# Performance work log

Hardware: AMD Instinct MI355X
Metric: run time of the kernel (lower is better)

The kernel has to match this reference:

```python
import jax, jax.numpy as jnp
import numpy as np
import math

N, E, LAT, MUL, HD = 20000, 160000, 128, 16, 32
H = LAT // HD          # 4 heads
D = 9                  # 0e+1o+2e spherical harmonics dim
SLICES = ((0, 1), (1, 4), (4, 9))
TPD = MUL * len(SLICES)


def _mlp(x, W1, b1, W2, b2):
    return jnp.dot(jax.nn.silu(jnp.dot(x, W1) + b1), W2) + b2


def _eq_linear(x, W):
    # block-diagonal per-l channel mixing: x [E, mul, D], W [n_l, mul, mul]
    return jnp.concatenate([jnp.einsum('ji,eim->ejm', W[l], x[:, :, s:t])
                            for l, (s, t) in enumerate(SLICES)], axis=-1)


def _residual(x, x_new, uc):
    co = jax.lax.rsqrt(uc * uc + 1.0)
    return co * x + (uc * co) * x_new


def _vec_rej(feat, dirs):
    d = dirs[:, None, :]
    return feat - (feat * d).sum(-1, keepdims=True) * d


def _so3_ln(x, eps=1e-8):
    # equivariant RMS layernorm per irrep block
    out = []
    for s, t in SLICES:
        blk = x[:, :, s:t]
        rms = jnp.sqrt((blk * blk).sum(-1).mean(-1) + eps)  # [N]
        out.append(blk / rms[:, None, None])
    return jnp.concatenate(out, axis=-1)


def _ln(x, g, b, eps=1e-5):
    mu = x.mean(-1, keepdims=True)
    var = ((x - mu) ** 2).mean(-1, keepdims=True)
    return (x - mu) * jax.lax.rsqrt(var + eps) * g + b


def _forward(h, X, t_ij, spharms, update_coeff, Wtq, Wtk, Wrs_W, Wrs_b, Wq_W, Wq_b, Wk_W, Wk_b, Wre_W, ln_g, ln_b, Wvu,
             gs_W1, gs_b1, gs_W2, gs_b2, gv_W1, gv_b1, gv_W2, gv_b2, gw_W1, gw_b1, gw_W2, gw_b2,
             gt_W1, gt_b1, gt_W2, gt_b2, gsp_W1, gsp_b1, gsp_W2, gsp_b2, md_W1, md_b1, md_W2, md_b2,
             mt_W1, mt_b1, mt_W2, mt_b2, gm_W1, gm_b1, gm_W2, gm_b2,
             edge_center, edge_neighbor, num_nodes):
    uc = update_coeff
    Xn = X[edge_neighbor]                                     # [E, mul, D]
    Xq = _vec_rej(_eq_linear(X[edge_center], Wtq), spharms)
    Xk = _vec_rej(_eq_linear(Xn, Wtk), -spharms)
    # CG scalar contraction (l x l -> 0e, uuu): normalized per-l dot product
    w = jnp.concatenate([(Xq[:, :, s:t] * Xk[:, :, s:t]).sum(-1) / math.sqrt(t - s)
                         for s, t in SLICES], axis=-1)        # [E, 3*mul]
    dt = _mlp(w, gw_W1, gw_b1, gw_W2, gw_b2) * _mlp(t_ij, gt_W1, gt_b1, gt_W2, gt_b2)
    t_ij = _residual(t_ij, dt, uc)
    h_i = h[edge_center]
    h_j = h[edge_neighbor]
    spatial = (t_ij @ Wrs_W + Wrs_b) * _mlp(h_j, gs_W1, gs_b1, gs_W2, gs_b2)
    En = t_ij.shape[0]
    q = (h_i @ Wq_W + Wq_b).reshape(En, H, HD)
    k = (h_j @ Wk_W + Wk_b).reshape(En, H, HD)
    v = _mlp(h_j, gv_W1, gv_b1, gv_W2, gv_b2)
    ta = jax.nn.silu(t_ij @ Wre_W).reshape(En, H, HD)
    alpha = (q * k * ta).sum(-1) / math.sqrt(HD)              # [E, H]
    amax = jax.ops.segment_max(alpha, edge_center, num_segments=num_nodes)
    ex = jnp.exp(alpha - amax[edge_center])
    den = jax.ops.segment_sum(ex, edge_center, num_segments=num_nodes)
    attn = ex / den[edge_center]                              # scatter_softmax
    sea = (attn[:, :, None] * v.reshape(En, H, HD)).reshape(En, LAT)
    combined = sea + spatial
    gates = _mlp(combined, gsp_W1, gsp_b1, gsp_W2, gsp_b2)
    o_s, o_d, o_t = gates[:, :LAT], gates[:, LAT:2 * LAT], gates[:, 2 * LAT:]
    dh = _ln(jax.ops.segment_sum(o_s, edge_center, num_segments=num_nodes), ln_g, ln_b)
    h = _residual(h, dh, uc)
    gd = _mlp(o_d, md_W1, md_b1, md_W2, md_b2)
    gtt = _mlp(o_t, mt_W1, mt_b1, mt_W2, mt_b2)
    dXij = gd[:, :, None] * spharms[:, None, :] + gtt[:, :, None] * Xn
    dX = _so3_ln(jax.ops.segment_sum(dXij, edge_center, num_segments=num_nodes))
    X = _residual(X, dX, uc)
    # EQFF
    Xp = jnp.einsum('nmi,mj->nji', X, Wvu)
    nrm = jnp.sqrt((Xp * Xp).sum(-1) + 1e-12)
    g = _mlp(jnp.concatenate([h, nrm], axis=-1), gm_W1, gm_b1, gm_W2, gm_b2)
    h = h + g[:, :LAT]
    X = X + g[:, LAT:, None] * Xp
    return h, X, t_ij


def setup_inputs() -> dict:
    key = jax.random.key(0)
    ks = jax.random.split(key, 24)

    def mk_mlp(k, din, dout):
        k1, k2 = jax.random.split(k)
        return (jax.random.normal(k1, (din, LAT)) / math.sqrt(din), jnp.zeros((LAT,)),
                jax.random.normal(k2, (LAT, dout)) / math.sqrt(LAT), jnp.zeros((dout,)))

    inp = {
        'h': jax.random.normal(ks[0], (N, LAT)),
        'X': jax.random.normal(ks[1], (N, MUL, D)),
        't_ij': jax.random.normal(ks[2], (E, LAT)),
        'spharms': jax.random.normal(ks[3], (E, D)),
        'update_coeff': jnp.ones((1,), dtype=jnp.float32),
        'Wtq': jax.random.normal(ks[4], (len(SLICES), MUL, MUL)) / math.sqrt(MUL),
        'Wtk': jax.random.normal(ks[5], (len(SLICES), MUL, MUL)) / math.sqrt(MUL),
        'Wrs_W': jax.random.normal(ks[6], (LAT, LAT)) / math.sqrt(LAT),
        'Wrs_b': jnp.zeros((LAT,)),
        'Wq_W': jax.random.normal(ks[7], (LAT, LAT)) / math.sqrt(LAT),
        'Wq_b': jnp.zeros((LAT,)),
        'Wk_W': jax.random.normal(ks[8], (LAT, LAT)) / math.sqrt(LAT),
        'Wk_b': jnp.zeros((LAT,)),
        'Wre_W': jax.random.normal(ks[9], (LAT, LAT)) / math.sqrt(LAT),
        'ln_g': jnp.ones((LAT,)),
        'ln_b': jnp.zeros((LAT,)),
        'Wvu': jax.random.normal(ks[10], (MUL, MUL)) / math.sqrt(MUL),
    }
    for name, din, dout, k in [('gs', LAT, LAT, ks[11]), ('gv', LAT, LAT, ks[12]), ('gw', TPD, LAT, ks[13]),
                               ('gt', LAT, LAT, ks[14]), ('gsp', LAT, 3 * LAT, ks[15]), ('md', LAT, MUL, ks[16]),
                               ('mt', LAT, MUL, ks[17]), ('gm', LAT + MUL, LAT + MUL, ks[18])]:
        W1, b1, W2, b2 = mk_mlp(k, din, dout)
        inp[name + '_W1'], inp[name + '_b1'], inp[name + '_W2'], inp[name + '_b2'] = W1, b1, W2, b2
    inp['edge_center'] = jax.random.randint(ks[19], (E,), 0, N)
    inp['edge_neighbor'] = jax.random.randint(ks[20], (E,), 0, N)
    inp['num_nodes'] = N
    return inp


def reference(h, X, t_ij, spharms, update_coeff, Wtq, Wtk, Wrs_W, Wrs_b, Wq_W, Wq_b, Wk_W, Wk_b, Wre_W, ln_g, ln_b, Wvu,
              gs_W1, gs_b1, gs_W2, gs_b2, gv_W1, gv_b1, gv_W2, gv_b2, gw_W1, gw_b1, gw_W2, gw_b2,
              gt_W1, gt_b1, gt_W2, gt_b2, gsp_W1, gsp_b1, gsp_W2, gsp_b2, md_W1, md_b1, md_W2, md_b2,
              mt_W1, mt_b1, mt_W2, mt_b2, gm_W1, gm_b1, gm_W2, gm_b2,
              edge_center, edge_neighbor, num_nodes):
    return _forward(h, X, t_ij, spharms, update_coeff, Wtq, Wtk, Wrs_W, Wrs_b, Wq_W, Wq_b, Wk_W, Wk_b, Wre_W, ln_g, ln_b, Wvu,
                    gs_W1, gs_b1, gs_W2, gs_b2, gv_W1, gv_b1, gv_W2, gv_b2, gw_W1, gw_b1, gw_W2, gw_b2,
                    gt_W1, gt_b1, gt_W2, gt_b2, gsp_W1, gsp_b1, gsp_W2, gsp_b2, md_W1, md_b1, md_W2, md_b2,
                    mt_W1, mt_b1, mt_W2, mt_b2, gm_W1, gm_b1, gm_W2, gm_b2,
                    edge_center, edge_neighbor, num_nodes)
```

## Files before the change

kernel.cpp:

```cpp
#include <hip/hip_runtime.h>
#include <math.h>

#define N_NODES 20000
#define E_EDGES 160000
#define LAT 128
#define MUL 16
#define DD 9
#define TPD 48

#define WS_QB     ((size_t)0)
#define WS_KB     (WS_QB + (size_t)N_NODES*LAT/2)
#define WS_VB     (WS_KB + (size_t)N_NODES*LAT/2)
#define WS_SB     (WS_VB + (size_t)N_NODES*LAT/2)
#define WS_W48    (WS_SB + (size_t)N_NODES*LAT/2)
#define WS_SPATB  (WS_W48 + (size_t)E_EDGES*TPD)
#define WS_ALPHA  (WS_SPATB + (size_t)E_EDGES*LAT/2)
#define WS_ZERO   (WS_ALPHA + (size_t)E_EDGES*4)
#define WS_AMAX   WS_ZERO
#define WS_DEN    (WS_AMAX + (size_t)N_NODES*4)
#define WS_HSUM   (WS_DEN + (size_t)N_NODES*4)
#define WS_NDX    (WS_HSUM + (size_t)N_NODES*LAT/2)
#define WS_END    (WS_NDX + (size_t)N_NODES*72)
#define ZERO_CNT  (WS_END - WS_ZERO)
#define WS_WB     WS_END
#define WS_XB     (WS_WB + (size_t)145408)

#define WOFF_WQ   0
#define WOFF_WK   16384
#define WOFF_GV1  32768
#define WOFF_GV2  49152
#define WOFF_GS1  65536
#define WOFF_GS2  81920
#define WOFF_GW1  98304
#define WOFF_GW2  106496
#define WOFF_GT1  122880
#define WOFF_GT2  139264
#define WOFF_WRS  155648
#define WOFF_WRE  172032
#define WOFF_GSP1 188416
#define WOFF_GSP2 204800
#define WOFF_MD1  253952
#define WOFF_MD2  270336
#define WOFF_MT1  272384
#define WOFF_MT2  288768
#define WB_TOTAL  290816

#define PREP_ZB   11250
#define PREP_PB   1136
#define PREP_XB   5625
#define K1B       (N_NODES/32)
#define K2B       (E_EDGES/16)

#define DEVI __device__ __forceinline__

typedef short short8 __attribute__((ext_vector_type(8)));
typedef float f32x4 __attribute__((ext_vector_type(4)));

DEVI float silu_f(float x){ return x / (1.f + __expf(-x)); }
DEVI unsigned int fmap(float x){ unsigned int b=__float_as_uint(x); return (b&0x80000000u)? ~b : (b|0x80000000u); }
DEVI float funmap(unsigned int u){ return (u&0x80000000u)? __uint_as_float(u&0x7fffffffu) : __uint_as_float(~u); }

DEVI unsigned short f2b(float f){ unsigned int u=__float_as_uint(f); return (unsigned short)((u + 0x7fffu + ((u>>16)&1u))>>16); }
DEVI unsigned int f2b2(float lo, float hi){ return ((unsigned int)f2b(hi)<<16) | (unsigned int)f2b(lo); }
DEVI float b2f(unsigned short u){ return __uint_as_float(((unsigned int)u)<<16); }

DEVI void atom_pk(unsigned short* p, unsigned int pk){
  asm volatile("global_atomic_pk_add_bf16 %0, %1, off" :: "v"(p), "v"(pk) : "memory");
}

DEVI f32x4 mfma16(short8 a, short8 b, f32x4 c){
  return __builtin_amdgcn_mfma_f32_16x16x32_bf16(a,b,c,0,0,0);
}

template<int KB>
DEVI void mm_tile2(const unsigned short* act, int strideUS, const unsigned short* Wp,
                   int ntile, int m, int quad, f32x4* acc){
  const unsigned short* wp = Wp + (size_t)ntile*KB*512 + (size_t)quad*128 + m*8;
  const unsigned short* a0 = act + m*strideUS + quad*8;
  const unsigned short* a1 = a0 + 16*strideUS;
  #pragma unroll
  for (int kb=0;kb<KB;++kb){
    short8 bfr = *(const short8*)(wp + (size_t)kb*512);
    short8 af0 = *(const short8*)(a0 + kb*32);
    short8 af1 = *(const short8*)(a1 + kb*32);
    acc[0]=mfma16(af0,bfr,acc[0]);
    acc[1]=mfma16(af1,bfr,acc[1]);
  }
}

template<int KB>
DEVI void mm_tile1(const unsigned short* act, int strideUS, const unsigned short* Wp,
                   int mtbase, int m, int quad, f32x4& acc){
  const unsigned short* wp = Wp + (size_t)quad*128 + m*8;
  const unsigned short* a0 = act + (mtbase*16+m)*strideUS + quad*8;
  #pragma unroll
  for (int kb=0;kb<KB;++kb){
    short8 bfr = *(const short8*)(wp + (size_t)kb*512);
    short8 af  = *(const short8*)(a0 + kb*32);
    acc=mfma16(af,bfr,acc);
  }
}

template<int R, int KD, int LDSTRIDE>
DEVI void mm_acc(const float* src, const float* __restrict__ W, int wstride, int t, float* acc){
  #pragma unroll 2
  for (int k=0;k<KD;k+=4){
    float4 xv[R];
    #pragma unroll
    for (int r=0;r<R;++r) xv[r] = *(const float4*)(src + r*LDSTRIDE + k);
    #pragma unroll
    for (int kk=0;kk<4;++kk){
      float wk = W[(size_t)(k+kk)*wstride + t];
      #pragma unroll
      for (int r=0;r<R;++r) acc[r] += ((const float*)&xv[r])[kk]*wk;
    }
  }
}

__global__ __launch_bounds__(256) void k_prep(
  const float* __restrict__ X,
  const float* __restrict__ Wq,const float* __restrict__ Wk,
  const float* __restrict__ gv1,const float* __restrict__ gv2,
  const float* __restrict__ gs1,const float* __restrict__ gs2,
  const float* __restrict__ gw1,const float* __restrict__ gw2,
  const float* __restrict__ gt1,const float* __restrict__ gt2,
  const float* __restrict__ Wrs,const float* __restrict__ Wre,
  const float* __restrict__ gsp1,const float* __restrict__ gsp2,
  const float* __restrict__ md1,const float* __restrict__ md2,
  const float* __restrict__ mt1,const float* __restrict__ mt2,
  float* __restrict__ ws)
{
  const int b = blockIdx.x, tid = threadIdx.x;
  if (b < PREP_ZB){
    size_t i = (size_t)b*256 + tid;
    if (i < ZERO_CNT) ws[WS_ZERO + i] = 0.f;
    return;
  }
  if (b < PREP_ZB + PREP_PB){
    int i = (b - PREP_ZB)*256 + tid;
    if (i >= WB_TOTAL) return;
    unsigned short* dst = (unsigned short*)(ws + WS_WB);
    const int off[19] = {0,16384,32768,49152,65536,81920,98304,106496,122880,139264,
                         155648,172032,188416,204800,253952,270336,272384,288768,290816};
    int mi=0;
    while (i >= off[mi+1]) ++mi;
    int li = i - off[mi];
    int N = (mi==13)?384:((mi==15||mi==17)?16:128);
    int Ksrc = (mi==6)?48:128;
    int KB = (mi==6)?2:4;
    int j = li&7; int t = li>>3;
    int n_in = t&15; t>>=4;
    int quad = t&3; t>>=2;
    int k_block = t % KB; int n_tile = t / KB;
    int k = k_block*32 + quad*8 + j;
    int n = n_tile*16 + n_in;
    const float* src;
    switch(mi){
      case 0: src=Wq; break;  case 1: src=Wk; break;
      case 2: src=gv1; break; case 3: src=gv2; break;
      case 4: src=gs1; break; case 5: src=gs2; break;
      case 6: src=gw1; break; case 7: src=gw2; break;
      case 8: src=gt1; break; case 9: src=gt2; break;
      case 10: src=Wrs; break; case 11: src=Wre; break;
      case 12: src=gsp1; break; case 13: src=gsp2; break;
      case 14: src=md1; break; case 15: src=md2; break;
      default: src=(mi==16)?mt1:mt2; break;
    }
    float v = (k < Ksrc) ? src[(size_t)k*N + n] : 0.f;
    dst[i] = f2b(v);
    return;
  }
  {
    size_t idx = (size_t)(b - PREP_ZB - PREP_PB)*256 + tid;
    if (idx < (size_t)N_NODES*72){
      float2 v = *(const float2*)(X + idx*2);
      ((unsigned int*)(ws + WS_XB))[idx] = f2b2(v.x, v.y);
    }
    return;
  }
}

__global__ __launch_bounds__(256) void k12_node_edge(
  const float* __restrict__ h, const float* __restrict__ sph,
  const float* __restrict__ Wtq, const float* __restrict__ Wtk,
  const int* __restrict__ ec, const int* __restrict__ en,
  const unsigned short* __restrict__ WB,
  const float* __restrict__ Wq_b,const float* __restrict__ Wk_b,
  const float* __restrict__ gv_b1,const float* __restrict__ gv_b2,
  const float* __restrict__ gs_b1,const float* __restrict__ gs_b2,
  float* __restrict__ ws)
{
  __shared__ __align__(16) unsigned short SH[8704];
  const int tid=threadIdx.x;
  if (blockIdx.x < K1B){
    unsigned short* B0 = SH;
    unsigned short* B1 = SH + 32*136;
    const int lane=tid&63, w=tid>>6, m=lane&15, quad=lane>>4;
    const int n0=blockIdx.x*32;
    for (int idx=tid; idx<1024; idx+=256){ int r=idx>>5, c4=(idx&31)*4;
      float4 hv = *(const float4*)(h+(size_t)(n0+r)*128+c4);
      *(unsigned int*)(B0+r*136+c4)   = f2b2(hv.x,hv.y);
      *(unsigned int*)(B0+r*136+c4+2) = f2b2(hv.z,hv.w); }
    __syncthreads();
    unsigned short* Qb=(unsigned short*)(ws+WS_QB);
    unsigned short* Kb=(unsigned short*)(ws+WS_KB);
    unsigned short* Vb=(unsigned short*)(ws+WS_VB);
    unsigned short* Sb=(unsigned short*)(ws+WS_SB);
    f32x4 z4 = {0.f,0.f,0.f,0.f};
    { f32x4 acc[2][2]={{z4,z4},{z4,z4}};
      #pragma unroll
      for(int i=0;i<2;++i) mm_tile2<4>(B0,136,WB+WOFF_WQ, w*2+i, m, quad, acc[i]);
      #pragma unroll
      for(int i=0;i<2;++i){ int col=(w*2+i)*16+m; float bv=Wq_b[col];
        #pragma unroll
        for(int mt=0;mt<2;++mt)
          #pragma unroll
          for(int r=0;r<4;++r){ int row=mt*16+quad*4+r;
            Qb[(size_t)(n0+row)*128+col]=f2b(acc[i][mt][r]+bv); } } }
    { f32x4 acc[2][2]={{z4,z4},{z4,z4}};
      #pragma unroll
      for(int i=0;i<2;++i) mm_tile2<4>(B0,136,WB+WOFF_WK, w*2+i, m, quad, acc[i]);
      #pragma unroll
      for(int i=0;i<2;++i){ int col=(w*2+i)*16+m; float bv=Wk_b[col];
        #pragma unroll
        for(int mt=0;mt<2;++mt)
          #pragma unroll
          for(int r=0;r<4;++r){ int row=mt*16+quad*4+r;
            Kb[(size_t)(n0+row)*128+col]=f2b(acc[i][mt][r]+bv); } } }
    { f32x4 acc[2][2]={{z4,z4},{z4,z4}};
      #pragma unroll
      for(int i=0;i<2;++i) mm_tile2<4>(B0,136,WB+WOFF_GV1, w*2+i, m, quad, acc[i]);
      #pragma unroll
      for(int i=0;i<2;++i){ int col=(w*2+i)*16+m; float bv=gv_b1[col];
        #pragma unroll
        for(int mt=0;mt<2;++mt)
          #pragma unroll
          for(int r=0;r<4;++r) B1[(mt*16+quad*4+r)*136+col]=f2b(silu_f(acc[i][mt][r]+bv)); } }
    __syncthreads();
    { f32x4 acc[2][2]={{z4,z4},{z4,z4}};
      #pragma unroll
      for(int i=0;i<2;++i) mm_tile2<4>(B1,136,WB+WOFF_GV2, w*2+i, m, quad, acc[i]);
      #pragma unroll
      for(int i=0;i<2;++i){ int col=(w*2+i)*16+m; float bv=gv_b2[col];
        #pragma unroll
        for(int mt=0;mt<2;++mt)
          #pragma unroll
          for(int r=0;r<4;++r){ int row=mt*16+quad*4+r;
            Vb[(size_t)(n0+row)*128+col]=f2b(acc[i][mt][r]+bv); } } }
    __syncthreads();
    { f32x4 acc[2][2]={{z4,z4},{z4,z4}};
      #pragma unroll
      for(int i=0;i<2;++i) mm_tile2<4>(B0,136,WB+WOFF_GS1, w*2+i, m, quad, acc[i]);
      #pragma unroll
      for(int i=0;i<2;++i){ int col=(w*2+i)*16+m; float bv=gs_b1[col];
        #pragma unroll
        for(int mt=0;mt<2;++mt)
          #pragma unroll
          for(int r=0;r<4;++r) B1[(mt*16+quad*4+r)*136+col]=f2b(silu_f(acc[i][mt][r]+bv)); } }
    __syncthreads();
    { f32x4 acc[2][2]={{z4,z4},{z4,z4}};
      #pragma unroll
      for(int i=0;i<2;++i) mm_tile2<4>(B1,136,WB+WOFF_GS2, w*2+i, m, quad, acc[i]);
      #pragma unroll
      for(int i=0;i<2;++i){ int col=(w*2+i)*16+m; float bv=gs_b2[col];
        #pragma unroll
        for(int mt=0;mt<2;++mt)
          #pragma unroll
          for(int r=0;r<4;++r){ int row=mt*16+quad*4+r;
            Sb[(size_t)(n0+row)*128+col]=f2b(acc[i][mt][r]+bv); } } }
    return;
  }
  {
    unsigned short* xcb = SH;
    unsigned short* xnb = SH + 2304;
    float* sphL = (float*)(SH + 4608);
    float* wq   = (float*)(SH + 4896);
    float* wkk  = (float*)(SH + 6432);
    int*   ceI  = (int*)(SH + 7968);
    int*   nbI  = (int*)(SH + 8032);
    const int e0=(blockIdx.x - K1B)*16;
    if (tid<16){ ceI[tid]=ec[e0+tid]; nbI[tid]=en[e0+tid]; }
    for (int idx=tid; idx<768; idx+=256){ wq[idx]=Wtq[idx]; wkk[idx]=Wtk[idx]; }
    __syncthreads();
    const unsigned short* Xb=(const unsigned short*)(ws+WS_XB);
    for (int idx=tid; idx<1152; idx+=256){ int r=idx/72, p=idx-r*72;
      *(unsigned int*)(xcb + r*144 + 2*p) = *(const unsigned int*)(Xb + (size_t)ceI[r]*144 + 2*p);
      *(unsigned int*)(xnb + r*144 + 2*p) = *(const unsigned int*)(Xb + (size_t)nbI[r]*144 + 2*p); }
    if (tid<144){ int r=tid/9,c=tid%9; sphL[r*9+c]=sph[(size_t)(e0+r)*9+c]; }
    __syncthreads();
    const int el=tid>>4, j=tid&15;
    float xq[9], xk[9];
    const int ss[3]={0,1,4}, se[3]={1,4,9};
    #pragma unroll
    for (int l=0;l<3;++l){
      for (int mm2=ss[l]; mm2<se[l]; ++mm2){
        float aq=0.f, ak=0.f;
        #pragma unroll
        for (int i=0;i<16;++i){
          float wql = wq[l*256 + j*16 + i], wkl = wkk[l*256 + j*16 + i];
          aq += wql*b2f(xcb[el*144 + i*9+mm2]);
          ak += wkl*b2f(xnb[el*144 + i*9+mm2]);
        }
        xq[mm2]=aq; xk[mm2]=ak;
      }
    }
    float dq=0.f, dk=0.f;
    #pragma unroll
    for (int d=0; d<9; ++d){ dq += xq[d]*sphL[el*9+d]; dk += xk[d]*sphL[el*9+d]; }
    #pragma unroll
    for (int d=0; d<9; ++d){ xq[d] -= dq*sphL[el*9+d]; xk[d] -= dk*sphL[el*9+d]; }
    const float isc[3] = {1.f, 0.5773502691896258f, 0.4472135954999579f};
    unsigned short* W48u = (unsigned short*)(ws+WS_W48);
    #pragma unroll
    for (int l=0;l<3;++l){
      float s=0.f;
      for (int mm2=ss[l]; mm2<se[l]; ++mm2) s += xq[mm2]*xk[mm2];
      W48u[(size_t)(e0+el)*TPD + l*16 + j] = f2b(s*isc[l]);
    }
    return;
  }
}

__global__ __launch_bounds__(256) void k3_edge_t(
  const float* __restrict__ t_in, const int* __restrict__ ec, const int* __restrict__ en,
  const unsigned short* __restrict__ WB,
  const float* __restrict__ gw_b1,const float* __restrict__ gw_b2,
  const float* __restrict__ gt_b1,const float* __restrict__ gt_b2,
  const float* __restrict__ Wrs_b,
  const float* __restrict__ ucp, float* __restrict__ ws, float* __restrict__ outT)
{
  __shared__ __align__(16) unsigned short tin_b[32*136], hid_b[32*136];
  __shared__ int ceI[32], nbI[32];
  const int tid=threadIdx.x, lane=tid&63, w=tid>>6, m=lane&15, quad=lane>>4;
  const int e0=blockIdx.x*32;
  if (tid<32){ ceI[tid]=ec[e0+tid]; nbI[tid]=en[e0+tid]; }
  for (int idx=tid; idx<1024; idx+=256){ int r=idx>>5, c4=(idx&31)*4;
    float4 tv = *(const float4*)(t_in+(size_t)(e0+r)*128+c4);
    *(unsigned int*)(tin_b+r*136+c4)   = f2b2(tv.x,tv.y);
    *(unsigned int*)(tin_b+r*136+c4+2) = f2b2(tv.z,tv.w); }
  const unsigned short* W48u=(const unsigned short*)(ws+WS_W48);
  short8 wfr[2][2];
  #pragma unroll
  for (int rr=0;rr<2;++rr){
    const unsigned short* base = W48u + (size_t)(e0 + rr*16 + m)*TPD;
    wfr[rr][0] = *(const short8*)(base + quad*8);
    if (quad<2) wfr[rr][1] = *(const short8*)(base + 32 + quad*8);
    else { short8 z = {0,0,0,0,0,0,0,0}; wfr[rr][1] = z; }
  }
  __syncthreads();
  const float uc=ucp[0], co=rsqrtf(uc*uc+1.f), ucco=uc*co;
  f32x4 z4 = {0.f,0.f,0.f,0.f};
  { f32x4 acc[2][2]={{z4,z4},{z4,z4}};
    #pragma unroll
    for(int i=0;i<2;++i){
      const unsigned short* wp = WB+WOFF_GW1 + (size_t)(w*2+i)*1024 + (size_t)quad*128 + m*8;
      #pragma unroll
      for(int kb=0;kb<2;++kb){
        short8 bfr = *(const short8*)(wp + (size_t)kb*512);
        acc[i][0]=mfma16(wfr[0][kb],bfr,acc[i][0]);
        acc[i][1]=mfma16(wfr[1][kb],bfr,acc[i][1]);
      }
    }
    #pragma unroll
    for(int i=0;i<2;++i){ int col=(w*2+i)*16+m; float bv=gw_b1[col];
      #pragma unroll
      for(int mt=0;mt<2;++mt)
        #pragma unroll
        for(int r=0;r<4;++r) hid_b[(mt*16+quad*4+r)*136+col]=f2b(silu_f(acc[i][mt][r]+bv)); } }
  __syncthreads();
  f32x4 accw[2][2]={{z4,z4},{z4,z4}};
  #pragma unroll
  for(int i=0;i<2;++i) mm_tile2<4>(hid_b,136,WB+WOFF_GW2, w*2+i, m, quad, accw[i]);
  __syncthreads();
  { f32x4 acc[2][2]={{z4,z4},{z4,z4}};
    #pragma unroll
    for(int i=0;i<2;++i) mm_tile2<4>(tin_b,136,WB+WOFF_GT1, w*2+i, m, quad, acc[i]);
    #pragma unroll
    for(int i=0;i<2;++i){ int col=(w*2+i)*16+m; float bv=gt_b1[col];
      #pragma unroll
      for(int mt=0;mt<2;++mt)
        #pragma unroll
        for(int r=0;r<4;++r) hid_b[(mt*16+quad*4+r)*136+col]=f2b(silu_f(acc[i][mt][r]+bv)); } }
  __syncthreads();
  { f32x4 acct[2][2]={{z4,z4},{z4,z4}};
    #pragma unroll
    for(int i=0;i<2;++i) mm_tile2<4>(hid_b,136,WB+WOFF_GT2, w*2+i, m, quad, acct[i]);
    #pragma unroll
    for(int i=0;i<2;++i){ int col=(w*2+i)*16+m; float bw=gw_b2[col], bt=gt_b2[col];
      #pragma unroll
      for(int mt=0;mt<2;++mt)
        #pragma unroll
        for(int r=0;r<4;++r){ int row=mt*16+quad*4+r;
          float dt=(accw[i][mt][r]+bw)*(acct[i][mt][r]+bt);
          float tn=co*b2f(tin_b[row*136+col]) + ucco*dt;
          tin_b[row*136+col]=f2b(tn);
          outT[(size_t)(e0+row)*128+col]=tn; } } }
  __syncthreads();
  unsigned short* spatB = (unsigned short*)(ws+WS_SPATB);
  const unsigned short* Sb=(const unsigned short*)(ws+WS_SB);
  { f32x4 acc[2][2]={{z4,z4},{z4,z4}};
    #pragma unroll
    for(int i=0;i<2;++i) mm_tile2<4>(tin_b,136,WB+WOFF_WRS, w*2+i, m, quad, acc[i]);
    #pragma unroll
    for(int i=0;i<2;++i){ int col=(w*2+i)*16+m; float bv=Wrs_b[col];
      #pragma unroll
      for(int mt=0;mt<2;++mt)
        #pragma unroll
        for(int r=0;r<4;++r){ int row=mt*16+quad*4+r;
          float sv=b2f(Sb[(size_t)nbI[row]*128+col]);
          spatB[(size_t)(e0+row)*128+col]=f2b((acc[i][mt][r]+bv)*sv); } } }
  { f32x4 acc[2][2]={{z4,z4},{z4,z4}};
    #pragma unroll
    for(int i=0;i<2;++i) mm_tile2<4>(tin_b,136,WB+WOFF_WRE, w*2+i, m, quad, acc[i]);
    const unsigned short* Qb=(const unsigned short*)(ws+WS_QB);
    const unsigned short* Kb=(const unsigned short*)(ws+WS_KB);
    unsigned int* amaxu=(unsigned int*)(ws+WS_AMAX);
    #pragma unroll
    for(int mt=0;mt<2;++mt)
      #pragma unroll
      for(int r=0;r<4;++r){ int row=mt*16+quad*4+r;
        int ce=ceI[row], nb=nbI[row];
        float p=0.f;
        #pragma unroll
        for(int i=0;i<2;++i){ int col=(w*2+i)*16+m;
          float qv=b2f(Qb[(size_t)ce*128+col]);
          float kv=b2f(Kb[(size_t)nb*128+col]);
          p += qv*kv*silu_f(acc[i][mt][r]); }
        p += __shfl_xor(p,1); p += __shfl_xor(p,2); p += __shfl_xor(p,4); p += __shfl_xor(p,8);
        if (m==0){
          float aval = p * 0.17677669529663687f;
          int e=e0+row;
          ws[WS_ALPHA+(size_t)e*4+w]=aval;
          atomicMax(&amaxu[(size_t)ce*4+w], fmap(aval));
        } } }
}

__global__ __launch_bounds__(256) void k4_softmax(const int* __restrict__ ec, float* __restrict__ ws){
  int i = blockIdx.x*256 + threadIdx.x;
  if (i >= E_EDGES*4) return;
  int e = i>>2, hh = i&3;
  int c = ec[e];
  float a = ws[WS_ALPHA + i];
  const unsigned int* amaxu = (const unsigned int*)(ws + WS_AMAX);
  float am = funmap(amaxu[(size_t)c*4+hh]);
  float exv = __expf(a - am);
  ws[WS_ALPHA + i] = exv;
  atomicAdd(&ws[WS_DEN + (size_t)c*4 + hh], exv);
}

__global__ __launch_bounds__(256) void k5_edge_gate(
  const float* __restrict__ sph,
  const int* __restrict__ ec, const int* __restrict__ en,
  const unsigned short* __restrict__ WB,
  const float* __restrict__ gsp_b1,const float* __restrict__ gsp_b2,
  const float* __restrict__ md_b1,const float* __restrict__ md_b2,
  const float* __restrict__ mt_b1,const float* __restrict__ mt_b2,
  float* __restrict__ ws)
{
  __shared__ __align__(16) unsigned short A[32*136], B[32*136], C[32*136];
  __shared__ float gdL[32*16], gtL[32*16], attnL[32*4];
  __shared__ int ceI[32], nbI[32];
  const int tid=threadIdx.x, lane=tid&63, w=tid>>6, m=lane&15, quad=lane>>4;
  const int e0=blockIdx.x*32;
  if (tid<32){ ceI[tid]=ec[e0+tid]; nbI[tid]=en[e0+tid]; }
  __syncthreads();
  if (tid<128){ int r=tid>>2, hh=tid&3;
    attnL[tid] = ws[WS_ALPHA+(size_t)(e0+r)*4+hh] / ws[WS_DEN+(size_t)ceI[r]*4+hh]; }
  __syncthreads();
  const unsigned short* Vb=(const unsigned short*)(ws+WS_VB);
  const unsigned short* spatB=(const unsigned short*)(ws+WS_SPATB);
  for (int idx=tid; idx<2048; idx+=256){ int r=idx>>6, c2=(idx&63)*2;
    unsigned int va = *(const unsigned int*)(Vb+(size_t)nbI[r]*128+c2);
    unsigned int sp = *(const unsigned int*)(spatB+(size_t)(e0+r)*128+c2);
    float a = attnL[r*4+(c2>>5)];
    float v0 = a*b2f((unsigned short)va) + b2f((unsigned short)sp);
    float v1 = a*b2f((unsigned short)(va>>16)) + b2f((unsigned short)(sp>>16));
    *(unsigned int*)(A+r*136+c2) = f2b2(v0,v1); }
  __syncthreads();
  f32x4 z4 = {0.f,0.f,0.f,0.f};
  { f32x4 acc[2][2]={{z4,z4},{z4,z4}};
    #pragma unroll
    for(int i=0;i<2;++i) mm_tile2<4>(A,136,WB+WOFF_GSP1, w*2+i, m, quad, acc[i]);
    #pragma unroll
    for(int i=0;i<2;++i){ int col=(w*2+i)*16+m; float bv=gsp_b1[col];
      #pragma unroll
      for(int mt=0;mt<2;++mt)
        #pragma unroll
        for(int r=0;r<4;++r) B[(mt*16+quad*4+r)*136+col]=f2b(silu_f(acc[i][mt][r]+bv)); } }
  __syncthreads();
  { f32x4 acc[3][2][2];
    #pragma unroll
    for(int g2=0;g2<3;++g2)
      #pragma unroll
      for(int i=0;i<2;++i){ acc[g2][i][0]=z4; acc[g2][i][1]=z4; }
    #pragma unroll
    for(int g2=0;g2<3;++g2)
      #pragma unroll
      for(int i=0;i<2;++i)
        mm_tile2<4>(B,136,WB+WOFF_GSP2, g2*8+w*2+i, m, quad, acc[g2][i]);
    unsigned short* hsumB=(unsigned short*)(ws+WS_HSUM);
    #pragma unroll
    for(int i=0;i<2;++i){ int col=(w*2+i)*16+m;
      float bS=gsp_b2[col], bD=gsp_b2[128+col], bT=gsp_b2[256+col];
      #pragma unroll
      for(int mt=0;mt<2;++mt)
        #pragma unroll
        for(int r=0;r<4;++r){ int row=mt*16+quad*4+r;
          float vS = acc[0][i][mt][r]+bS;
          float vO = __shfl_xor(vS,1);
          if(!(m&1)){
            atom_pk(hsumB + (size_t)ceI[row]*128 + col, f2b2(vS,vO));
          }
          A[row*136+col]=f2b(acc[1][i][mt][r]+bD);
          C[row*136+col]=f2b(acc[2][i][mt][r]+bT); } } }
  __syncthreads();
  { f32x4 acc[2][2]={{z4,z4},{z4,z4}};
    #pragma unroll
    for(int i=0;i<2;++i) mm_tile2<4>(A,136,WB+WOFF_MD1, w*2+i, m, quad, acc[i]);
    #pragma unroll
    for(int i=0;i<2;++i){ int col=(w*2+i)*16+m; float bv=md_b1[col];
      #pragma unroll
      for(int mt=0;mt<2;++mt)
        #pragma unroll
        for(int r=0;r<4;++r) B[(mt*16+quad*4+r)*136+col]=f2b(silu_f(acc[i][mt][r]+bv)); } }
  __syncthreads();
  { f32x4 acc[2][2]={{z4,z4},{z4,z4}};
    #pragma unroll
    for(int i=0;i<2;++i) mm_tile2<4>(C,136,WB+WOFF_MT1, w*2+i, m, quad, acc[i]);
    #pragma unroll
    for(int i=0;i<2;++i){ int col=(w*2+i)*16+m; float bv=mt_b1[col];
      #pragma unroll
      for(int mt=0;mt<2;++mt)
        #pragma unroll
        for(int r=0;r<4;++r) A[(mt*16+quad*4+r)*136+col]=f2b(silu_f(acc[i][mt][r]+bv)); } }
  __syncthreads();
  { if (w<2){
      f32x4 a=z4; mm_tile1<4>(B,136,WB+WOFF_MD2, w, m, quad, a);
      #pragma unroll
      for(int r=0;r<4;++r) gdL[(w*16+quad*4+r)*16+m]=a[r]+md_b2[m];
    } else {
      f32x4 a=z4; mm_tile1<4>(A,136,WB+WOFF_MT2, w-2, m, quad, a);
      #pragma unroll
      for(int r=0;r<4;++r) gtL[((w-2)*16+quad*4+r)*16+m]=a[r]+mt_b2[m];
    } }
  __syncthreads();
  unsigned short* ndxB=(unsigned short*)(ws+WS_NDX);
  const unsigned short* Xb=(const unsigned short*)(ws+WS_XB);
  for (int idx=tid; idx<2304; idx+=256){
    int r=idx/72, p=idx-r*72; int c0=2*p, c1=c0+1;
    int mm0=c0/9, d0=c0-mm0*9;
    int mm1=c1/9, d1=c1-mm1*9;
    const float* sphE = sph + (size_t)(e0+r)*9;
    unsigned int xa = *(const unsigned int*)(Xb + (size_t)nbI[r]*144 + c0);
    float x0=b2f((unsigned short)xa), x1=b2f((unsigned short)(xa>>16));
    float v0 = gdL[r*16+mm0]*sphE[d0] + gtL[r*16+mm0]*x0;
    float v1 = gdL[r*16+mm1]*sphE[d1] + gtL[r*16+mm1]*x1;
    atom_pk(ndxB + (size_t)ceI[r]*144 + c0, f2b2(v0,v1));
  }
}

__global__ __launch_bounds__(128) void k6_node(
  const float* __restrict__ h, const float* __restrict__ Xin,
  const float* __restrict__ ln_g,const float* __restrict__ ln_b,
  const float* __restrict__ Wvu,
  const float* __restrict__ gm_W1,const float* __restrict__ gm_b1,
  const float* __restrict__ gm_W2,const float* __restrict__ gm_b2,
  const float* __restrict__ ucp, const float* __restrict__ ws,
  float* __restrict__ outH, float* __restrict__ outX)
{
  __shared__ float cat[4][144], dxb[4][144], xnw[4][144], xp[4][144], hid[4][LAT];
  __shared__ float red[4][2][2], rinv[4][3], gX[4][16], wvu[256];
  const int t=threadIdx.x, n0=blockIdx.x*4;
  const unsigned short* hsumB=(const unsigned short*)(ws+WS_HSUM);
  const unsigned short* ndxB =(const unsigned short*)(ws+WS_NDX);
  const float uc=ucp[0], co=rsqrtf(uc*uc+1.f), ucco=uc*co;
  for (int idx=t; idx<256; idx+=128) wvu[idx]=Wvu[idx];
  for (int idx=t; idx<576; idx+=128){ int r=idx/144,c=idx%144; dxb[r][c]=b2f(ndxB[(size_t)(n0+r)*144+c]); }
  float xv_[4];
  #pragma unroll
  for (int r=0;r<4;++r){
    float x=b2f(hsumB[(size_t)(n0+r)*LAT+t]); xv_[r]=x;
    float s=x, ss=x*x;
    for (int off=32; off; off>>=1){ s+=__shfl_down(s,off,64); ss+=__shfl_down(ss,off,64); }
    if ((t&63)==0){ red[r][t>>6][0]=s; red[r][t>>6][1]=ss; }
  }
  __syncthreads();
  #pragma unroll
  for (int r=0;r<4;++r){
    float s=red[r][0][0]+red[r][1][0], ss=red[r][0][1]+red[r][1][1];
    float mu=s*(1.f/128.f), var=ss*(1.f/128.f)-mu*mu;
    float dh=(xv_[r]-mu)*rsqrtf(var+1e-5f)*ln_g[t]+ln_b[t];
    cat[r][t]=co*h[(size_t)(n0+r)*LAT+t]+ucco*dh;
  }
  if (t<12){
    int r=t/3, l=t-r*3;
    int s0 = (l==0)?0:((l==1)?1:4);
    int s1 = (l==0)?1:((l==1)?4:9);
    float sum=0.f;
    for (int mm2=0;mm2<16;++mm2)
      for (int d=s0;d<s1;++d){ float v=dxb[r][mm2*9+d]; sum+=v*v; }
    rinv[r][l]=rsqrtf(sum*(1.f/16.f)+1e-8f);
  }
  __syncthreads();
  for (int idx=t; idx<144; idx+=128){
    int d=idx%9; int l=(d==0)?0:((d<4)?1:2);
    #pragma unroll
    for (int r=0;r<4;++r)
      xnw[r][idx]=co*Xin[(size_t)(n0+r)*144+idx]+ucco*dxb[r][idx]*rinv[r][l];
  }
  __syncthreads();
  for (int idx=t; idx<144; idx+=128){
    int j=idx/9, i=idx-j*9;
    #pragma unroll
    for (int r=0;r<4;++r){
      float a=0.f;
      #pragma unroll
      for (int mm2=0;mm2<16;++mm2) a+=xnw[r][mm2*9+i]*wvu[mm2*16+j];
      xp[r][idx]=a;
    }
  }
  __syncthreads();
  if (t<64){ int r=t>>4, j=t&15; float s=1e-12f;
    #pragma unroll
    for (int i=0;i<9;++i){ float v=xp[r][j*9+i]; s+=v*v; }
    cat[r][128+j]=sqrtf(s); }
  __syncthreads();
  { float acc[4]; float b=gm_b1[t];
    #pragma unroll
    for(int r=0;r<4;++r)acc[r]=b;
    mm_acc<4,144,144>(&cat[0][0],gm_W1,LAT,t,acc);
    #pragma unroll
    for(int r=0;r<4;++r) hid[r][t]=silu_f(acc[r]); }
  __syncthreads();
  { float acc[4]; float b=gm_b2[t];
    #pragma unroll
    for(int r=0;r<4;++r)acc[r]=b;
    mm_acc<4,LAT,LAT>(&hid[0][0],gm_W2,144,t,acc);
    #pragma unroll
    for(int r=0;r<4;++r) outH[(size_t)(n0+r)*LAT+t]=cat[r][t]+acc[r]; }
  if (t<16){ float acc[4]; float b=gm_b2[128+t];
    #pragma unroll
    for(int r=0;r<4;++r)acc[r]=b;
    for (int k=0;k<LAT;++k){ float wk=gm_W2[(size_t)k*144+128+t];
      #pragma unroll
      for(int r=0;r<4;++r) acc[r]+=hid[r][k]*wk; }
    #pragma unroll
    for(int r=0;r<4;++r) gX[r][t]=acc[r]; }
  __syncthreads();
  for (int idx=t; idx<144; idx+=128){
    int j=idx/9;
    #pragma unroll
    for (int r=0;r<4;++r)
      outX[(size_t)(n0+r)*144+idx]=xnw[r][idx]+gX[r][j]*xp[r][idx];
  }
}

extern "C" void kernel_launch(void* const* d_in, const int* in_sizes, int n_in,
                              void* d_out, int out_size, void* d_ws, size_t ws_size,
                              hipStream_t stream)
{
  const float* h      = (const float*)d_in[0];
  const float* X      = (const float*)d_in[1];
  const float* t_ij   = (const float*)d_in[2];
  const float* sph    = (const float*)d_in[3];
  const float* ucp    = (const float*)d_in[4];
  const float* Wtq    = (const float*)d_in[5];
  const float* Wtk    = (const float*)d_in[6];
  const float* Wrs_W  = (const float*)d_in[7];
  const float* Wrs_b  = (const float*)d_in[8];
  const float* Wq_W   = (const float*)d_in[9];
  const float* Wq_b   = (const float*)d_in[10];
  const float* Wk_W   = (const float*)d_in[11];
  const float* Wk_b   = (const float*)d_in[12];
  const float* Wre_W  = (const float*)d_in[13];
  const float* ln_g   = (const float*)d_in[14];
  const float* ln_b   = (const float*)d_in[15];
  const float* Wvu    = (const float*)d_in[16];
  const float* gs_W1=(const float*)d_in[17], *gs_b1=(const float*)d_in[18],
             *gs_W2=(const float*)d_in[19], *gs_b2=(const float*)d_in[20];
  const float* gv_W1=(const float*)d_in[21], *gv_b1=(const float*)d_in[22],
             *gv_W2=(const float*)d_in[23], *gv_b2=(const float*)d_in[24];
  const float* gw_W1=(const float*)d_in[25], *gw_b1=(const float*)d_in[26],
             *gw_W2=(const float*)d_in[27], *gw_b2=(const float*)d_in[28];
  const float* gt_W1=(const float*)d_in[29], *gt_b1=(const float*)d_in[30],
             *gt_W2=(const float*)d_in[31], *gt_b2=(const float*)d_in[32];
  const float* gsp_W1=(const float*)d_in[33], *gsp_b1=(const float*)d_in[34],
             *gsp_W2=(const float*)d_in[35], *gsp_b2=(const float*)d_in[36];
  const float* md_W1=(const float*)d_in[37], *md_b1=(const float*)d_in[38],
             *md_W2=(const float*)d_in[39], *md_b2=(const float*)d_in[40];
  const float* mt_W1=(const float*)d_in[41], *mt_b1=(const float*)d_in[42],
             *mt_W2=(const float*)d_in[43], *mt_b2=(const float*)d_in[44];
  const float* gm_W1=(const float*)d_in[45], *gm_b1=(const float*)d_in[46],
             *gm_W2=(const float*)d_in[47], *gm_b2=(const float*)d_in[48];
  const int* ec = (const int*)d_in[49];
  const int* en = (const int*)d_in[50];
  (void)in_sizes; (void)n_in; (void)out_size; (void)ws_size;

  float* ws   = (float*)d_ws;
  unsigned short* WB = (unsigned short*)(ws + WS_WB);
  float* outH = (float*)d_out;
  float* outX = outH + (size_t)N_NODES*LAT;
  float* outT = outX + (size_t)N_NODES*MUL*DD;

  k_prep<<<dim3(PREP_ZB + PREP_PB + PREP_XB), dim3(256), 0, stream>>>(
      X, Wq_W,Wk_W, gv_W1,gv_W2, gs_W1,gs_W2, gw_W1,gw_W2, gt_W1,gt_W2,
      Wrs_W,Wre_W, gsp_W1,gsp_W2, md_W1,md_W2, mt_W1,mt_W2, ws);
  k12_node_edge<<<dim3(K1B + K2B), dim3(256), 0, stream>>>(
      h, sph, Wtq, Wtk, ec, en, WB, Wq_b, Wk_b, gv_b1,gv_b2, gs_b1,gs_b2, ws);
  k3_edge_t<<<dim3(E_EDGES/32), dim3(256), 0, stream>>>(t_ij, ec, en, WB,
      gw_b1,gw_b2, gt_b1,gt_b2, Wrs_b, ucp, ws, outT);
  k4_softmax<<<dim3((E_EDGES*4)/256), dim3(256), 0, stream>>>(ec, ws);
  k5_edge_gate<<<dim3(E_EDGES/32), dim3(256), 0, stream>>>(sph, ec, en, WB,
      gsp_b1,gsp_b2, md_b1,md_b2, mt_b1,mt_b2, ws);
  k6_node<<<dim3(N_NODES/4), dim3(128), 0, stream>>>(h, X, ln_g, ln_b, Wvu,
      gm_W1,gm_b1,gm_W2,gm_b2, ucp, ws, outH, outX);
}
```

Measured before the change: 897.7 us.

## Split fused node/edge kernel and interleave gw/gt MLP chains in edge-t kernel

Splits the combined node-projection and edge-contraction kernel into two separate launches, so each gets its own shared-memory footprint and register allocation instead of both sharing the larger union. In k3, the gw and gt MLP first layers are computed together into two separate hidden buffers, then both second-layer matmuls run in one phase. This cuts the barrier count and lets the MFMA chains overlap. The cost is an extra kernel launch, more LDS per block in k3 (a third 32x136 buffer) and more live accumulators, which may reduce occupancy.

```diff
diff --git a/kernel.cpp b/kernel.cpp
--- a/kernel.cpp
+++ b/kernel.cpp
@@ -48,8 +48,6 @@
 #define PREP_ZB   11250
 #define PREP_PB   1136
 #define PREP_XB   5625
-#define K1B       (N_NODES/32)
-#define K2B       (E_EDGES/16)
 
 #define DEVI __device__ __forceinline__
 
@@ -180,144 +178,136 @@
   }
 }
 
-__global__ __launch_bounds__(256) void k12_node_edge(
-  const float* __restrict__ h, const float* __restrict__ sph,
-  const float* __restrict__ Wtq, const float* __restrict__ Wtk,
-  const int* __restrict__ ec, const int* __restrict__ en,
+__global__ __launch_bounds__(256) void k1_node(const float* __restrict__ h,
   const unsigned short* __restrict__ WB,
   const float* __restrict__ Wq_b,const float* __restrict__ Wk_b,
   const float* __restrict__ gv_b1,const float* __restrict__ gv_b2,
   const float* __restrict__ gs_b1,const float* __restrict__ gs_b2,
   float* __restrict__ ws)
 {
-  __shared__ __align__(16) unsigned short SH[8704];
-  const int tid=threadIdx.x;
-  if (blockIdx.x < K1B){
-    unsigned short* B0 = SH;
-    unsigned short* B1 = SH + 32*136;
-    const int lane=tid&63, w=tid>>6, m=lane&15, quad=lane>>4;
-    const int n0=blockIdx.x*32;
-    for (int idx=tid; idx<1024; idx+=256){ int r=idx>>5, c4=(idx&31)*4;
-      float4 hv = *(const float4*)(h+(size_t)(n0+r)*128+c4);
-      *(unsigned int*)(B0+r*136+c4)   = f2b2(hv.x,hv.y);
-      *(unsigned int*)(B0+r*136+c4+2) = f2b2(hv.z,hv.w); }
-    __syncthreads();
-    unsigned short* Qb=(unsigned short*)(ws+WS_QB);
-    unsigned short* Kb=(unsigned short*)(ws+WS_KB);
-    unsigned short* Vb=(unsigned short*)(ws+WS_VB);
-    unsigned short* Sb=(unsigned short*)(ws+WS_SB);
-    f32x4 z4 = {0.f,0.f,0.f,0.f};
-    { f32x4 acc[2][2]={{z4,z4},{z4,z4}};
-      #pragma unroll
-      for(int i=0;i<2;++i) mm_tile2<4>(B0,136,WB+WOFF_WQ, w*2+i, m, quad, acc[i]);
-      #pragma unroll
-      for(int i=0;i<2;++i){ int col=(w*2+i)*16+m; float bv=Wq_b[col];
-        #pragma unroll
-        for(int mt=0;mt<2;++mt)
-          #pragma unroll
-          for(int r=0;r<4;++r){ int row=mt*16+quad*4+r;
-            Qb[(size_t)(n0+row)*128+col]=f2b(acc[i][mt][r]+bv); } } }
-    { f32x4 acc[2][2]={{z4,z4},{z4,z4}};
-      #pragma unroll
-      for(int i=0;i<2;++i) mm_tile2<4>(B0,136,WB+WOFF_WK, w*2+i, m, quad, acc[i]);
-      #pragma unroll
-      for(int i=0;i<2;++i){ int col=(w*2+i)*16+m; float bv=Wk_b[col];
-        #pragma unroll
-        for(int mt=0;mt<2;++mt)
-          #pragma unroll
-          for(int r=0;r<4;++r){ int row=mt*16+quad*4+r;
-            Kb[(size_t)(n0+row)*128+col]=f2b(acc[i][mt][r]+bv); } } }
-    { f32x4 acc[2][2]={{z4,z4},{z4,z4}};
-      #pragma unroll
-      for(int i=0;i<2;++i) mm_tile2<4>(B0,136,WB+WOFF_GV1, w*2+i, m, quad, acc[i]);
-      #pragma unroll
-      for(int i=0;i<2;++i){ int col=(w*2+i)*16+m; float bv=gv_b1[col];
-        #pragma unroll
-        for(int mt=0;mt<2;++mt)
-          #pragma unroll
-          for(int r=0;r<4;++r) B1[(mt*16+quad*4+r)*136+col]=f2b(silu_f(acc[i][mt][r]+bv)); } }
-    __syncthreads();
-    { f32x4 acc[2][2]={{z4,z4},{z4,z4}};
-      #pragma unroll
-      for(int i=0;i<2;++i) mm_tile2<4>(B1,136,WB+WOFF_GV2, w*2+i, m, quad, acc[i]);
-      #pragma unroll
-      for(int i=0;i<2;++i){ int col=(w*2+i)*16+m; float bv=gv_b2[col];
-        #pragma unroll
-        for(int mt=0;mt<2;++mt)
-          #pragma unroll
-          for(int r=0;r<4;++r){ int row=mt*16+quad*4+r;
-            Vb[(size_t)(n0+row)*128+col]=f2b(acc[i][mt][r]+bv); } } }
-    __syncthreads();
-    { f32x4 acc[2][2]={{z4,z4},{z4,z4}};
-      #pragma unroll
-      for(int i=0;i<2;++i) mm_tile2<4>(B0,136,WB+WOFF_GS1, w*2+i, m, quad, acc[i]);
-      #pragma unroll
-      for(int i=0;i<2;++i){ int col=(w*2+i)*16+m; float bv=gs_b1[col];
-        #pragma unroll
-        for(int mt=0;mt<2;++mt)
-          #pragma unroll
-          for(int r=0;r<4;++r) B1[(mt*16+quad*4+r)*136+col]=f2b(silu_f(acc[i][mt][r]+bv)); } }
-    __syncthreads();
-    { f32x4 acc[2][2]={{z4,z4},{z4,z4}};
-      #pragma unroll
-      for(int i=0;i<2;++i) mm_tile2<4>(B1,136,WB+WOFF_GS2, w*2+i, m, quad, acc[i]);
-      #pragma unroll
-      for(int i=0;i<2;++i){ int col=(w*2+i)*16+m; float bv=gs_b2[col];
-        #pragma unroll
-        for(int mt=0;mt<2;++mt)
-          #pragma unroll
-          for(int r=0;r<4;++r){ int row=mt*16+quad*4+r;
-            Sb[(size_t)(n0+row)*128+col]=f2b(acc[i][mt][r]+bv); } } }
-    return;
-  }
-  {
-    unsigned short* xcb = SH;
-    unsigned short* xnb = SH + 2304;
-    float* sphL = (float*)(SH + 4608);
-    float* wq   = (float*)(SH + 4896);
-    float* wkk  = (float*)(SH + 6432);
-    int*   ceI  = (int*)(SH + 7968);
-    int*   nbI  = (int*)(SH + 8032);
-    const int e0=(blockIdx.x - K1B)*16;
-    if (tid<16){ ceI[tid]=ec[e0+tid]; nbI[tid]=en[e0+tid]; }
-    for (int idx=tid; idx<768; idx+=256){ wq[idx]=Wtq[idx]; wkk[idx]=Wtk[idx]; }
-    __syncthreads();
-    const unsigned short* Xb=(const unsigned short*)(ws+WS_XB);
-    for (int idx=tid; idx<1152; idx+=256){ int r=idx/72, p=idx-r*72;
-      *(unsigned int*)(xcb + r*144 + 2*p) = *(const unsigned int*)(Xb + (size_t)ceI[r]*144 + 2*p);
-      *(unsigned int*)(xnb + r*144 + 2*p) = *(const unsigned int*)(Xb + (size_t)nbI[r]*144 + 2*p); }
-    if (tid<144){ int r=tid/9,c=tid%9; sphL[r*9+c]=sph[(size_t)(e0+r)*9+c]; }
-    __syncthreads();
-    const int el=tid>>4, j=tid&15;
-    float xq[9], xk[9];
-    const int ss[3]={0,1,4}, se[3]={1,4,9};
-    #pragma unroll
-    for (int l=0;l<3;++l){
-      for (int mm2=ss[l]; mm2<se[l]; ++mm2){
-        float aq=0.f, ak=0.f;
-        #pragma unroll
-        for (int i=0;i<16;++i){
-          float wql = wq[l*256 + j*16 + i], wkl = wkk[l*256 + j*16 + i];
-          aq += wql*b2f(xcb[el*144 + i*9+mm2]);
-          ak += wkl*b2f(xnb[el*144 + i*9+mm2]);
-        }
-        xq[mm2]=aq; xk[mm2]=ak;
+  __shared__ __align__(16) unsigned short B0[32*136], B1[32*136];
+  const int tid=threadIdx.x, lane=tid&63, w=tid>>6, m=lane&15, quad=lane>>4;
+  const int n0=blockIdx.x*32;
+  for (int idx=tid; idx<1024; idx+=256){ int r=idx>>5, c4=(idx&31)*4;
+    float4 hv = *(const float4*)(h+(size_t)(n0+r)*128+c4);
+    *(unsigned int*)(B0+r*136+c4)   = f2b2(hv.x,hv.y);
+    *(unsigned int*)(B0+r*136+c4+2) = f2b2(hv.z,hv.w); }
+  __syncthreads();
+  unsigned short* Qb=(unsigned short*)(ws+WS_QB);
+  unsigned short* Kb=(unsigned short*)(ws+WS_KB);
+  unsigned short* Vb=(unsigned short*)(ws+WS_VB);
+  unsigned short* Sb=(unsigned short*)(ws+WS_SB);
+  f32x4 z4 = {0.f,0.f,0.f,0.f};
+  { f32x4 acc[2][2]={{z4,z4},{z4,z4}};
+    #pragma unroll
+    for(int i=0;i<2;++i) mm_tile2<4>(B0,136,WB+WOFF_WQ, w*2+i, m, quad, acc[i]);
+    #pragma unroll
+    for(int i=0;i<2;++i){ int col=(w*2+i)*16+m; float bv=Wq_b[col];
+      #pragma unroll
+      for(int mt=0;mt<2;++mt)
+        #pragma unroll
+        for(int r=0;r<4;++r){ int row=mt*16+quad*4+r;
+          Qb[(size_t)(n0+row)*128+col]=f2b(acc[i][mt][r]+bv); } } }
+  { f32x4 acc[2][2]={{z4,z4},{z4,z4}};
+    #pragma unroll
+    for(int i=0;i<2;++i) mm_tile2<4>(B0,136,WB+WOFF_WK, w*2+i, m, quad, acc[i]);
+    #pragma unroll
+    for(int i=0;i<2;++i){ int col=(w*2+i)*16+m; float bv=Wk_b[col];
+      #pragma unroll
+      for(int mt=0;mt<2;++mt)
+        #pragma unroll
+        for(int r=0;r<4;++r){ int row=mt*16+quad*4+r;
+          Kb[(size_t)(n0+row)*128+col]=f2b(acc[i][mt][r]+bv); } } }
+  { f32x4 acc[2][2]={{z4,z4},{z4,z4}};
+    #pragma unroll
+    for(int i=0;i<2;++i) mm_tile2<4>(B0,136,WB+WOFF_GV1, w*2+i, m, quad, acc[i]);
+    #pragma unroll
+    for(int i=0;i<2;++i){ int col=(w*2+i)*16+m; float bv=gv_b1[col];
+      #pragma unroll
+      for(int mt=0;mt<2;++mt)
+        #pragma unroll
+        for(int r=0;r<4;++r) B1[(mt*16+quad*4+r)*136+col]=f2b(silu_f(acc[i][mt][r]+bv)); } }
+  __syncthreads();
+  { f32x4 acc[2][2]={{z4,z4},{z4,z4}};
+    #pragma unroll
+    for(int i=0;i<2;++i) mm_tile2<4>(B1,136,WB+WOFF_GV2, w*2+i, m, quad, acc[i]);
+    #pragma unroll
+    for(int i=0;i<2;++i){ int col=(w*2+i)*16+m; float bv=gv_b2[col];
+      #pragma unroll
+      for(int mt=0;mt<2;++mt)
+        #pragma unroll
+        for(int r=0;r<4;++r){ int row=mt*16+quad*4+r;
+          Vb[(size_t)(n0+row)*128+col]=f2b(acc[i][mt][r]+bv); } } }
+  __syncthreads();
+  { f32x4 acc[2][2]={{z4,z4},{z4,z4}};
+    #pragma unroll
+    for(int i=0;i<2;++i) mm_tile2<4>(B0,136,WB+WOFF_GS1, w*2+i, m, quad, acc[i]);
+    #pragma unroll
+    for(int i=0;i<2;++i){ int col=(w*2+i)*16+m; float bv=gs_b1[col];
+      #pragma unroll
+      for(int mt=0;mt<2;++mt)
+        #pragma unroll
+        for(int r=0;r<4;++r) B1[(mt*16+quad*4+r)*136+col]=f2b(silu_f(acc[i][mt][r]+bv)); } }
+  __syncthreads();
+  { f32x4 acc[2][2]={{z4,z4},{z4,z4}};
+    #pragma unroll
+    for(int i=0;i<2;++i) mm_tile2<4>(B1,136,WB+WOFF_GS2, w*2+i, m, quad, acc[i]);
+    #pragma unroll
+    for(int i=0;i<2;++i){ int col=(w*2+i)*16+m; float bv=gs_b2[col];
+      #pragma unroll
+      for(int mt=0;mt<2;++mt)
+        #pragma unroll
+        for(int r=0;r<4;++r){ int row=mt*16+quad*4+r;
+          Sb[(size_t)(n0+row)*128+col]=f2b(acc[i][mt][r]+bv); } } }
+}
+
+__global__ __launch_bounds__(256) void k2_edge_w(
+  const float* __restrict__ sph,
+  const float* __restrict__ Wtq, const float* __restrict__ Wtk,
+  const int* __restrict__ ec, const int* __restrict__ en, float* __restrict__ ws)
+{
+  __shared__ unsigned short xcb[16*144], xnb[16*144];
+  __shared__ float sphL[16][9];
+  __shared__ float wq[768], wkk[768];
+  __shared__ int ceI[16], nbI[16];
+  const int tid=threadIdx.x, e0=blockIdx.x*16;
+  if (tid<16){ ceI[tid]=ec[e0+tid]; nbI[tid]=en[e0+tid]; }
+  for (int idx=tid; idx<768; idx+=256){ wq[idx]=Wtq[idx]; wkk[idx]=Wtk[idx]; }
+  __syncthreads();
+  const unsigned short* Xb=(const unsigned short*)(ws+WS_XB);
+  for (int idx=tid; idx<1152; idx+=256){ int r=idx/72, p=idx-r*72;
+    *(unsigned int*)(xcb + r*144 + 2*p) = *(const unsigned int*)(Xb + (size_t)ceI[r]*144 + 2*p);
+    *(unsigned int*)(xnb + r*144 + 2*p) = *(const unsigned int*)(Xb + (size_t)nbI[r]*144 + 2*p); }
+  if (tid<144){ int r=tid/9,c=tid%9; sphL[r][c]=sph[(size_t)(e0+r)*9+c]; }
+  __syncthreads();
+  const int el=tid>>4, j=tid&15;
+  float xq[9], xk[9];
+  const int ss[3]={0,1,4}, se[3]={1,4,9};
+  #pragma unroll
+  for (int l=0;l<3;++l){
+    for (int mm2=ss[l]; mm2<se[l]; ++mm2){
+      float aq=0.f, ak=0.f;
+      #pragma unroll
+      for (int i=0;i<16;++i){
+        float wql = wq[l*256 + j*16 + i], wkl = wkk[l*256 + j*16 + i];
+        aq += wql*b2f(xcb[el*144 + i*9+mm2]);
+        ak += wkl*b2f(xnb[el*144 + i*9+mm2]);
       }
+      xq[mm2]=aq; xk[mm2]=ak;
     }
-    float dq=0.f, dk=0.f;
-    #pragma unroll
-    for (int d=0; d<9; ++d){ dq += xq[d]*sphL[el*9+d]; dk += xk[d]*sphL[el*9+d]; }
-    #pragma unroll
-    for (int d=0; d<9; ++d){ xq[d] -= dq*sphL[el*9+d]; xk[d] -= dk*sphL[el*9+d]; }
-    const float isc[3] = {1.f, 0.5773502691896258f, 0.4472135954999579f};
-    unsigned short* W48u = (unsigned short*)(ws+WS_W48);
-    #pragma unroll
-    for (int l=0;l<3;++l){
-      float s=0.f;
-      for (int mm2=ss[l]; mm2<se[l]; ++mm2) s += xq[mm2]*xk[mm2];
-      W48u[(size_t)(e0+el)*TPD + l*16 + j] = f2b(s*isc[l]);
-    }
-    return;
+  }
+  float dq=0.f, dk=0.f;
+  #pragma unroll
+  for (int d=0; d<9; ++d){ dq += xq[d]*sphL[el][d]; dk += xk[d]*sphL[el][d]; }
+  #pragma unroll
+  for (int d=0; d<9; ++d){ xq[d] -= dq*sphL[el][d]; xk[d] -= dk*sphL[el][d]; }
+  const float isc[3] = {1.f, 0.5773502691896258f, 0.4472135954999579f};
+  unsigned short* W48u = (unsigned short*)(ws+WS_W48);
+  #pragma unroll
+  for (int l=0;l<3;++l){
+    float s=0.f;
+    for (int mm2=ss[l]; mm2<se[l]; ++mm2) s += xq[mm2]*xk[mm2];
+    W48u[(size_t)(e0+el)*TPD + l*16 + j] = f2b(s*isc[l]);
   }
 }
 
@@ -329,7 +319,7 @@
   const float* __restrict__ Wrs_b,
   const float* __restrict__ ucp, float* __restrict__ ws, float* __restrict__ outT)
 {
-  __shared__ __align__(16) unsigned short tin_b[32*136], hid_b[32*136];
+  __shared__ __align__(16) unsigned short tin_b[32*136], H1[32*136], H2[32*136];
   __shared__ int ceI[32], nbI[32];
   const int tid=threadIdx.x, lane=tid&63, w=tid>>6, m=lane&15, quad=lane>>4;
   const int e0=blockIdx.x*32;
@@ -350,41 +340,34 @@
   __syncthreads();
   const float uc=ucp[0], co=rsqrtf(uc*uc+1.f), ucco=uc*co;
   f32x4 z4 = {0.f,0.f,0.f,0.f};
-  { f32x4 acc[2][2]={{z4,z4},{z4,z4}};
+  { f32x4 accg[2][2]={{z4,z4},{z4,z4}};
     #pragma unroll
     for(int i=0;i<2;++i){
       const unsigned short* wp = WB+WOFF_GW1 + (size_t)(w*2+i)*1024 + (size_t)quad*128 + m*8;
       #pragma unroll
       for(int kb=0;kb<2;++kb){
         short8 bfr = *(const short8*)(wp + (size_t)kb*512);
-        acc[i][0]=mfma16(wfr[0][kb],bfr,acc[i][0]);
-        acc[i][1]=mfma16(wfr[1][kb],bfr,acc[i][1]);
+        accg[i][0]=mfma16(wfr[0][kb],bfr,accg[i][0]);
+        accg[i][1]=mfma16(wfr[1][kb],bfr,accg[i][1]);
       }
     }
-    #pragma unroll
-    for(int i=0;i<2;++i){ int col=(w*2+i)*16+m; float bv=gw_b1[col];
-      #pragma unroll
-      for(int mt=0;mt<2;++mt)
-        #pragma unroll
-        for(int r=0;r<4;++r) hid_b[(mt*16+quad*4+r)*136+col]=f2b(silu_f(acc[i][mt][r]+bv)); } }
-  __syncthreads();
-  f32x4 accw[2][2]={{z4,z4},{z4,z4}};
-  #pragma unroll
-  for(int i=0;i<2;++i) mm_tile2<4>(hid_b,136,WB+WOFF_GW2, w*2+i, m, quad, accw[i]);
-  __syncthreads();
-  { f32x4 acc[2][2]={{z4,z4},{z4,z4}};
-    #pragma unroll
-    for(int i=0;i<2;++i) mm_tile2<4>(tin_b,136,WB+WOFF_GT1, w*2+i, m, quad, acc[i]);
-    #pragma unroll
-    for(int i=0;i<2;++i){ int col=(w*2+i)*16+m; float bv=gt_b1[col];
-      #pragma unroll
-      for(int mt=0;mt<2;++mt)
-        #pragma unroll
-        for(int r=0;r<4;++r) hid_b[(mt*16+quad*4+r)*136+col]=f2b(silu_f(acc[i][mt][r]+bv)); } }
-  __syncthreads();
-  { f32x4 acct[2][2]={{z4,z4},{z4,z4}};
-    #pragma unroll
-    for(int i=0;i<2;++i) mm_tile2<4>(hid_b,136,WB+WOFF_GT2, w*2+i, m, quad, acct[i]);
+    f32x4 acct[2][2]={{z4,z4},{z4,z4}};
+    #pragma unroll
+    for(int i=0;i<2;++i) mm_tile2<4>(tin_b,136,WB+WOFF_GT1, w*2+i, m, quad, acct[i]);
+    #pragma unroll
+    for(int i=0;i<2;++i){ int col=(w*2+i)*16+m; float bg=gw_b1[col], bt=gt_b1[col];
+      #pragma unroll
+      for(int mt=0;mt<2;++mt)
+        #pragma unroll
+        for(int r=0;r<4;++r){ int row=mt*16+quad*4+r;
+          H1[row*136+col]=f2b(silu_f(accg[i][mt][r]+bg));
+          H2[row*136+col]=f2b(silu_f(acct[i][mt][r]+bt)); } } }
+  __syncthreads();
+  { f32x4 accw[2][2]={{z4,z4},{z4,z4}};
+    f32x4 acct[2][2]={{z4,z4},{z4,z4}};
+    #pragma unroll
+    for(int i=0;i<2;++i){ mm_tile2<4>(H1,136,WB+WOFF_GW2, w*2+i, m, quad, accw[i]);
+                          mm_tile2<4>(H2,136,WB+WOFF_GT2, w*2+i, m, quad, acct[i]); }
     #pragma unroll
     for(int i=0;i<2;++i){ int col=(w*2+i)*16+m; float bw=gw_b2[col], bt=gt_b2[col];
       #pragma unroll
@@ -705,8 +688,9 @@
   k_prep<<<dim3(PREP_ZB + PREP_PB + PREP_XB), dim3(256), 0, stream>>>(
       X, Wq_W,Wk_W, gv_W1,gv_W2, gs_W1,gs_W2, gw_W1,gw_W2, gt_W1,gt_W2,
       Wrs_W,Wre_W, gsp_W1,gsp_W2, md_W1,md_W2, mt_W1,mt_W2, ws);
-  k12_node_edge<<<dim3(K1B + K2B), dim3(256), 0, stream>>>(
-      h, sph, Wtq, Wtk, ec, en, WB, Wq_b, Wk_b, gv_b1,gv_b2, gs_b1,gs_b2, ws);
+  k1_node<<<dim3(N_NODES/32), dim3(256), 0, stream>>>(h, WB, Wq_b, Wk_b,
+      gv_b1,gv_b2, gs_b1,gs_b2, ws);
+  k2_edge_w<<<dim3(E_EDGES/16), dim3(256), 0, stream>>>(sph, Wtq, Wtk, ec, en, ws);
   k3_edge_t<<<dim3(E_EDGES/32), dim3(256), 0, stream>>>(t_ij, ec, en, WB,
       gw_b1,gw_b2, gt_b1,gt_b2, Wrs_b, ucp, ws, outT);
   k4_softmax<<<dim3((E_EDGES*4)/256), dim3(256), 0, stream>>>(ec, ws);
```

New measurement: 763.1 us. 15.0% less time.
